# Kernel optimization log

Hardware: AMD Instinct MI355X
Metric: run time of the kernel (lower is better)

Reference implementation:

```python
import jax, jax.numpy as jnp
import numpy as np

B, T, D, H = 4, 4096, 1024, 1024

def log_g(x):
    # log of g(x) = where(x>=0, x+0.5, sigmoid(x)), computed stably in log-space
    return jnp.where(x >= 0, jnp.log(jax.nn.relu(x) + 0.5), -jax.nn.softplus(-x))

def setup_inputs() -> dict:
    key = jax.random.key(0)
    ks = jax.random.split(key, 8)
    s = 1.0 / np.sqrt(D)
    return {
        "x":   jax.random.normal(ks[0], (B, T, D), dtype=jnp.float32),
        "h_0": jax.random.normal(ks[1], (B, H),    dtype=jnp.float32),
        "Wf":  jax.random.uniform(ks[2], (H, D), minval=-s, maxval=s, dtype=jnp.float32),
        "bf":  jax.random.uniform(ks[3], (H,),   minval=-s, maxval=s, dtype=jnp.float32),
        "Wi":  jax.random.uniform(ks[4], (H, D), minval=-s, maxval=s, dtype=jnp.float32),
        "bi":  jax.random.uniform(ks[5], (H,),   minval=-s, maxval=s, dtype=jnp.float32),
        "Wh":  jax.random.uniform(ks[6], (H, D), minval=-s, maxval=s, dtype=jnp.float32),
        "bh":  jax.random.uniform(ks[7], (H,),   minval=-s, maxval=s, dtype=jnp.float32),
    }

def reference(x, h_0, Wf, bf, Wi, bi, Wh, bh):
    # Gate pre-activations: (B, T, H)
    zf = jnp.einsum('btd,hd->bth', x, Wf) + bf
    zi = jnp.einsum('btd,hd->bth', x, Wi) + bi
    zh = jnp.einsum('btd,hd->bth', x, Wh) + bh

    # Normalized gates in log space: log f' = -softplus(diff), log i' = -softplus(-diff)
    diff = jax.nn.softplus(-zf) - jax.nn.softplus(-zi)
    log_f = -jax.nn.softplus(diff)
    log_i = -jax.nn.softplus(-diff)
    log_tilde_h = log_g(zh)

    log_h0 = log_g(h_0)[:, None, :]                               # (B, 1, H)
    log_values = jnp.concatenate([log_h0, log_i + log_tilde_h], axis=1)  # (B, T+1, H)

    # Log-space parallel scan: h_t = f_t h_{t-1} + v_t
    a_star = jnp.cumsum(log_f, axis=1)                            # (B, T, H)
    a_star_pad = jnp.pad(a_star, ((0, 0), (1, 0), (0, 0)))        # (B, T+1, H)
    log_h = a_star_pad + jax.lax.cumlogsumexp(log_values - a_star_pad, axis=1)
    return jnp.exp(log_h[:, 1:, :])                               # (B, T, H)
```

## Files before the change

kernel.cpp:

```cpp
#include <hip/hip_runtime.h>
#include <stdint.h>

#define BB 4
#define TT 4096
#define DD 1024
#define HH 1024
#define MM (BB * TT)
#define NC 128
#define CL (TT / NC)

typedef __bf16 bf16x8 __attribute__((ext_vector_type(8)));
typedef short  s16x8  __attribute__((ext_vector_type(8)));
typedef float  f32x4  __attribute__((ext_vector_type(4)));
typedef float  f32x16 __attribute__((ext_vector_type(16)));


__device__ __forceinline__ unsigned short f2bf(float f) {
    unsigned u = __float_as_uint(f);
    u += 0x7fffu + ((u >> 16) & 1u);
    return (unsigned short)(u >> 16);
}

__device__ __forceinline__ float bf2f(unsigned short u) {
    return __uint_as_float(((unsigned)u) << 16);
}

__device__ __forceinline__ float g_fn(float x) {
    return (x >= 0.f) ? (x + 0.5f) : 1.0f / (1.0f + __expf(-x));
}

__device__ __forceinline__ f32x16 mfma32(s16x8 a, s16x8 b, f32x16 c) {
    return __builtin_amdgcn_mfma_f32_32x32x16_bf16(
        __builtin_bit_cast(bf16x8, a), __builtin_bit_cast(bf16x8, b), c, 0, 0, 0);
}

__device__ __forceinline__ void async_copy16(const void* gsrc, void* ldst) {
    __builtin_amdgcn_global_load_lds(
        reinterpret_cast<__attribute__((address_space(1))) unsigned int*>(
            reinterpret_cast<uintptr_t>(gsrc)),
        reinterpret_cast<__attribute__((address_space(3))) unsigned int*>(
            reinterpret_cast<uintptr_t>(ldst)),
        16, 0, 0);
}


__global__ void cast_all(const float* __restrict__ x,
                         const float* __restrict__ Wf,
                         const float* __restrict__ Wi,
                         const float* __restrict__ Wh,
                         unsigned short* __restrict__ xb,
                         unsigned short* __restrict__ Wb) {
    const int NX = MM * DD / 4;
    int i = blockIdx.x * 256 + threadIdx.x;
    if (i < NX) {
        float4 v = reinterpret_cast<const float4*>(x)[i];
        ushort4 o;
        o.x = f2bf(v.x); o.y = f2bf(v.y); o.z = f2bf(v.z); o.w = f2bf(v.w);
        reinterpret_cast<ushort4*>(xb)[i] = o;
    } else {
        int j = i - NX;
        if (j < 3 * 262144) {
            int which = j >> 18, k = j & 262143;
            const float* s = (which == 0) ? Wf : ((which == 1) ? Wi : Wh);
            float4 v = reinterpret_cast<const float4*>(s)[k];
            ushort4 o;
            o.x = f2bf(v.x); o.y = f2bf(v.y); o.z = f2bf(v.z); o.w = f2bf(v.w);
            reinterpret_cast<ushort4*>(Wb)[(which << 18) + k] = o;
        }
    }
}


#define ISSUE(NB) do {                                                        \
    _Pragma("unroll")                                                         \
    for (int j = 0; j < 4; ++j)                                               \
        async_copy16(sbA[j] + voff, smem + (NB) * 16384 + ldsA[j]);           \
    _Pragma("unroll")                                                         \
    for (int j = 0; j < 3; ++j)                                               \
        async_copy16(sbB[j] + voff, smem + 32768 + (NB) * 12288 + ldsB[j]);   \
    voff += 32;                                                               \
} while (0)

#define COMPUTE(CB) do {                                                      \
    const char* Ab = smem + (CB) * 16384;                                     \
    const char* Bb = smem + 32768 + (CB) * 12288;                             \
    _Pragma("unroll")                                                         \
    for (int ks = 0; ks < 2; ++ks) {                                          \
        const int col = c0 ^ (ks << 5);                                       \
        s16x8 a0 = *reinterpret_cast<const s16x8*>(Ab + arowb + col);         \
        s16x8 a1 = *reinterpret_cast<const s16x8*>(Ab + arowb + 2048 + col);  \
        s16x8 a2 = *reinterpret_cast<const s16x8*>(Ab + arowb + 4096 + col);  \
        s16x8 a3 = *reinterpret_cast<const s16x8*>(Ab + arowb + 6144 + col);  \
        s16x8 b0 = *reinterpret_cast<const s16x8*>(Bb + browb + col);         \
        s16x8 b1 = *reinterpret_cast<const s16x8*>(Bb + browb + 4096 + col);  \
        s16x8 b2 = *reinterpret_cast<const s16x8*>(Bb + browb + 8192 + col);  \
        acc[0][0] = mfma32(a0, b0, acc[0][0]);                                \
        acc[1][0] = mfma32(a0, b1, acc[1][0]);                                \
        acc[2][0] = mfma32(a0, b2, acc[2][0]);                                \
        acc[0][1] = mfma32(a1, b0, acc[0][1]);                                \
        acc[1][1] = mfma32(a1, b1, acc[1][1]);                                \
        acc[2][1] = mfma32(a1, b2, acc[2][1]);                                \
        acc[0][2] = mfma32(a2, b0, acc[0][2]);                                \
        acc[1][2] = mfma32(a2, b1, acc[1][2]);                                \
        acc[2][2] = mfma32(a2, b2, acc[2][2]);                                \
        acc[0][3] = mfma32(a3, b0, acc[0][3]);                                \
        acc[1][3] = mfma32(a3, b1, acc[1][3]);                                \
        acc[2][3] = mfma32(a3, b2, acc[2][3]);                                \
    }                                                                         \
} while (0)

#define STEP(CB, NB, LAST) do {                                               \
    if (!(LAST)) {                                                            \
        ISSUE(NB);                                                            \
        asm volatile("s_waitcnt vmcnt(7)" ::: "memory");                      \
    } else {                                                                  \
        asm volatile("s_waitcnt vmcnt(0)" ::: "memory");                      \
    }                                                                         \
    __builtin_amdgcn_s_barrier();                                             \
    COMPUTE(CB);                                                              \
    asm volatile("s_waitcnt lgkmcnt(0)" ::: "memory");                        \
    __builtin_amdgcn_s_barrier();                                             \
} while (0)

__global__ __launch_bounds__(256, 2) void gemm_gates(
    const unsigned short* __restrict__ xb,
    const unsigned short* __restrict__ Wb,
    const float* __restrict__ bf_p, const float* __restrict__ bi_p,
    const float* __restrict__ bh_p,
    unsigned short* __restrict__ F, unsigned short* __restrict__ V) {
    __shared__ char smem[57344];

    const int tid  = threadIdx.x;
    const int lane = tid & 63;
    const int wub  = __builtin_amdgcn_readfirstlane(tid >> 6);

    const int bi  = blockIdx.x;
    const int xcd = bi & 7;
    const int jj  = bi >> 3;
    const int bm  = ((jj & 7) << 3) | xcd;
    const int bh  = jj >> 3;

    const int pm   = wub >> 1;
    const int ph   = wub & 1;

    int voff = (lane >> 2) * DD +
               (((lane & 3) ^ ((lane >> 3) & 3) ^ ((lane >> 5) & 1)) << 3);

    const unsigned short* sbA[4];
    const unsigned short* sbB[3];
    int ldsA[4], ldsB[3];
#pragma unroll
    for (int j = 0; j < 4; ++j) {
        int s = wub + j * 4;
        sbA[j]  = xb + (size_t)(bm * 256 + s * 16) * DD;
        ldsA[j] = s * 1024;
    }
#pragma unroll
    for (int j = 0; j < 3; ++j) {
        int s = wub + j * 4;
        sbB[j]  = Wb + (size_t)((s >> 2) * HH + bh * 64 + (s & 3) * 16) * DD;
        ldsB[j] = s * 1024;
    }

    const int c0 = ((((lane >> 5) & 1) ^ ((lane >> 1) & 3) ^ ((lane >> 3) & 1)) << 4);
    const int arowb = (pm * 128 + (lane & 31)) * 64;
    const int browb = (ph * 32 + (lane & 31)) * 64;

    f32x16 acc[3][4];
#pragma unroll
    for (int g = 0; g < 3; ++g)
#pragma unroll
        for (int mt = 0; mt < 4; ++mt)
            acc[g][mt] = (f32x16)(0.f);

    ISSUE(0);
    for (int t = 0; t < 15; ++t) {
        STEP(0, 1, 0);
        STEP(1, 0, 0);
    }
    STEP(0, 1, 0);
    STEP(1, 0, 1);

    const int h   = bh * 64 + ph * 32 + (lane & 31);
    const float bfs = bf_p[h], bis = bi_p[h], bhs = bh_p[h];
    const int mb  = bm * 256 + pm * 128 + ((lane >> 5) << 2);
#pragma unroll
    for (int mt = 0; mt < 4; ++mt) {
#pragma unroll
        for (int r = 0; r < 16; ++r) {
            const int m = mb + mt * 32 + (r & 3) + ((r >> 2) << 3);
            float zf = acc[0][mt][r] + bfs;
            float zi = acc[1][mt][r] + bis;
            float zh = acc[2][mt][r] + bhs;
            float ea = __expf(fminf(-zf, 60.f));
            float eb = __expf(fminf(-zi, 60.f));
            float s  = __builtin_amdgcn_rcpf(2.f + ea + eb);
            float fv = (1.f + eb) * s;
            float iv = (1.f + ea) * s;
            float gg = (zh >= 0.f) ? (zh + 0.5f)
                                   : __builtin_amdgcn_rcpf(1.f + __expf(-zh));
            size_t o = (size_t)m * HH + h;
            F[o] = f2bf(fv);
            V[o] = f2bf(iv * gg);
        }
    }
}


__global__ void scan1_kernel(const unsigned short* __restrict__ F,
                             const unsigned short* __restrict__ V,
                             float* __restrict__ Fc, float* __restrict__ Vc) {
    const int bx = blockIdx.x, tid = threadIdx.x;
    const int c = bx & (NC - 1), b = bx >> 7;
    const ushort4* F4 = (const ushort4*)F;
    const ushort4* V4 = (const ushort4*)V;
    size_t base = ((size_t)(b * TT + c * CL) * HH) / 4 + tid;
    float4 Fp = {1.f, 1.f, 1.f, 1.f}, hv = {0.f, 0.f, 0.f, 0.f};
#pragma unroll 8
    for (int s = 0; s < CL; ++s) {
        ushort4 fu = F4[base + (size_t)s * (HH / 4)];
        ushort4 vu = V4[base + (size_t)s * (HH / 4)];
        hv.x = fmaf(bf2f(fu.x), hv.x, bf2f(vu.x)); Fp.x *= bf2f(fu.x);
        hv.y = fmaf(bf2f(fu.y), hv.y, bf2f(vu.y)); Fp.y *= bf2f(fu.y);
        hv.z = fmaf(bf2f(fu.z), hv.z, bf2f(vu.z)); Fp.z *= bf2f(fu.z);
        hv.w = fmaf(bf2f(fu.w), hv.w, bf2f(vu.w)); Fp.w *= bf2f(fu.w);
    }
    size_t ci = ((size_t)(b * NC + c) * HH) / 4 + tid;
    ((float4*)Fc)[ci] = Fp;
    ((float4*)Vc)[ci] = hv;
}

__global__ void scan2_kernel(const float* __restrict__ h0,
                             const float* __restrict__ Fc,
                             const float* __restrict__ Vc,
                             float* __restrict__ Hin) {
    const int gid = blockIdx.x * 256 + threadIdx.x;
    const int b = gid >> 10, h = gid & (HH - 1);
    float carry = g_fn(h0[gid]);
#pragma unroll 8
    for (int c = 0; c < NC; ++c) {
        int ci = (b * NC + c) * HH + h;
        Hin[ci] = carry;
        carry = fmaf(Fc[ci], carry, Vc[ci]);
    }
}

__global__ void scan3_kernel(const unsigned short* __restrict__ F,
                             const unsigned short* __restrict__ V,
                             const float* __restrict__ Hin,
                             float* __restrict__ Out) {
    const int bx = blockIdx.x, tid = threadIdx.x;
    const int c = bx & (NC - 1), b = bx >> 7;
    const ushort4* F4 = (const ushort4*)F;
    const ushort4* V4 = (const ushort4*)V;
    float4* O4 = (float4*)Out;
    size_t base = ((size_t)(b * TT + c * CL) * HH) / 4 + tid;
    size_t ci = ((size_t)(b * NC + c) * HH) / 4 + tid;
    float4 carry = ((const float4*)Hin)[ci];
#pragma unroll 8
    for (int s = 0; s < CL; ++s) {
        size_t idx = base + (size_t)s * (HH / 4);
        ushort4 fu = F4[idx];
        ushort4 vu = V4[idx];
        carry.x = fmaf(bf2f(fu.x), carry.x, bf2f(vu.x));
        carry.y = fmaf(bf2f(fu.y), carry.y, bf2f(vu.y));
        carry.z = fmaf(bf2f(fu.z), carry.z, bf2f(vu.z));
        carry.w = fmaf(bf2f(fu.w), carry.w, bf2f(vu.w));
        O4[idx] = carry;
    }
}


extern "C" void kernel_launch(void* const* d_in, const int* in_sizes, int n_in,
                              void* d_out, int out_size, void* d_ws, size_t ws_size,
                              hipStream_t stream) {
    const float* x   = (const float*)d_in[0];
    const float* h0  = (const float*)d_in[1];
    const float* Wf  = (const float*)d_in[2];
    const float* bfp = (const float*)d_in[3];
    const float* Wi  = (const float*)d_in[4];
    const float* bip = (const float*)d_in[5];
    const float* Wh  = (const float*)d_in[6];
    const float* bhp = (const float*)d_in[7];
    float* out = (float*)d_out;

    char* ws = (char*)d_ws;
    unsigned short* xb = (unsigned short*)ws;
    unsigned short* Wb = (unsigned short*)(ws + 33554432);
    unsigned short* Fb = (unsigned short*)(ws + 39845888);
    unsigned short* Vb = (unsigned short*)(ws + 73400320);
    float* Fc  = (float*)(ws);
    float* Vc  = (float*)(ws + 2097152);
    float* Hin = (float*)(ws + 4194304);

    cast_all<<<19456, 256, 0, stream>>>(x, Wf, Wi, Wh, xb, Wb);
    gemm_gates<<<1024, 256, 0, stream>>>(xb, Wb, bfp, bip, bhp, Fb, Vb);
    scan1_kernel<<<BB * NC, 256, 0, stream>>>(Fb, Vb, Fc, Vc);
    scan2_kernel<<<16, 256, 0, stream>>>(h0, Fc, Vc, Hin);
    scan3_kernel<<<BB * NC, 256, 0, stream>>>(Fb, Vb, Hin, out);
}
```

Baseline: 285.7 us.

## Load weight fragments directly from global memory in MFMA-ready layout, bypassing LDS

The bf16 conversion kernel now writes the three weight matrices in a pre-swizzled layout matching the MFMA B-operand fragment order. The GEMM kernel loads B fragments straight from global memory into registers each k-step instead of staging them through shared memory. This cuts LDS traffic and footprint (57KB down to 32KB), which may allow more occupancy. The cost is more per-wave global/L2 loads of the weights (duplicated across waves) and changed vmcnt accounting, which risks stalls if latency is not hidden.

```diff
diff --git a/kernel.cpp b/kernel.cpp
--- a/kernel.cpp
+++ b/kernel.cpp
@@ -65,7 +65,11 @@
             float4 v = reinterpret_cast<const float4*>(s)[k];
             ushort4 o;
             o.x = f2bf(v.x); o.y = f2bf(v.y); o.z = f2bf(v.z); o.w = f2bf(v.w);
-            reinterpret_cast<ushort4*>(Wb)[(which << 18) + k] = o;
+            int E = k << 2;
+            int h = E >> 10, d = E & 1023;
+            int kb = d >> 5, q = (d >> 3) & 3, e = d & 7;
+            int off = kb * 98304 + q * 24576 + which * 8192 + h * 8 + e;
+            reinterpret_cast<ushort4*>(Wb)[off >> 2] = o;
         }
     }
 }
@@ -75,49 +79,49 @@
     _Pragma("unroll")                                                         \
     for (int j = 0; j < 4; ++j)                                               \
         async_copy16(sbA[j] + voff, smem + (NB) * 16384 + ldsA[j]);           \
-    _Pragma("unroll")                                                         \
-    for (int j = 0; j < 3; ++j)                                               \
-        async_copy16(sbB[j] + voff, smem + 32768 + (NB) * 12288 + ldsB[j]);   \
     voff += 32;                                                               \
 } while (0)
 
-#define COMPUTE(CB) do {                                                      \
-    const char* Ab = smem + (CB) * 16384;                                     \
-    const char* Bb = smem + 32768 + (CB) * 12288;                             \
+#define STEP(CB, NB, LAST) do {                                               \
+    s16x8 bq[2][3];                                                           \
     _Pragma("unroll")                                                         \
-    for (int ks = 0; ks < 2; ++ks) {                                          \
-        const int col = c0 ^ (ks << 5);                                       \
-        s16x8 a0 = *reinterpret_cast<const s16x8*>(Ab + arowb + col);         \
-        s16x8 a1 = *reinterpret_cast<const s16x8*>(Ab + arowb + 2048 + col);  \
-        s16x8 a2 = *reinterpret_cast<const s16x8*>(Ab + arowb + 4096 + col);  \
-        s16x8 a3 = *reinterpret_cast<const s16x8*>(Ab + arowb + 6144 + col);  \
-        s16x8 b0 = *reinterpret_cast<const s16x8*>(Bb + browb + col);         \
-        s16x8 b1 = *reinterpret_cast<const s16x8*>(Bb + browb + 4096 + col);  \
-        s16x8 b2 = *reinterpret_cast<const s16x8*>(Bb + browb + 8192 + col);  \
-        acc[0][0] = mfma32(a0, b0, acc[0][0]);                                \
-        acc[1][0] = mfma32(a0, b1, acc[1][0]);                                \
-        acc[2][0] = mfma32(a0, b2, acc[2][0]);                                \
-        acc[0][1] = mfma32(a1, b0, acc[0][1]);                                \
-        acc[1][1] = mfma32(a1, b1, acc[1][1]);                                \
-        acc[2][1] = mfma32(a1, b2, acc[2][1]);                                \
-        acc[0][2] = mfma32(a2, b0, acc[0][2]);                                \
-        acc[1][2] = mfma32(a2, b1, acc[1][2]);                                \
-        acc[2][2] = mfma32(a2, b2, acc[2][2]);                                \
-        acc[0][3] = mfma32(a3, b0, acc[0][3]);                                \
-        acc[1][3] = mfma32(a3, b1, acc[1][3]);                                \
-        acc[2][3] = mfma32(a3, b2, acc[2][3]);                                \
-    }                                                                         \
-} while (0)
-
-#define STEP(CB, NB, LAST) do {                                               \
+    for (int ks = 0; ks < 2; ++ks)                                            \
+        _Pragma("unroll")                                                     \
+        for (int g = 0; g < 3; ++g)                                           \
+            bq[ks][g] = *reinterpret_cast<const s16x8*>(                      \
+                wp + ks * 49152 + g * 8192);                                  \
+    wp += 98304;                                                              \
+    asm volatile("" ::: "memory");            \
     if (!(LAST)) {                                                            \
         ISSUE(NB);                                                            \
-        asm volatile("s_waitcnt vmcnt(7)" ::: "memory");                      \
+        asm volatile("s_waitcnt vmcnt(10)" ::: "memory");                     \
     } else {                                                                  \
-        asm volatile("s_waitcnt vmcnt(0)" ::: "memory");                      \
+        asm volatile("s_waitcnt vmcnt(6)" ::: "memory");                      \
     }                                                                         \
     __builtin_amdgcn_s_barrier();                                             \
-    COMPUTE(CB);                                                              \
+    {                                                                         \
+        const char* Ab = smem + (CB) * 16384;                                 \
+        _Pragma("unroll")                                                     \
+        for (int ks = 0; ks < 2; ++ks) {                                      \
+            const int col = c0 ^ (ks << 5);                                   \
+            s16x8 a0 = *reinterpret_cast<const s16x8*>(Ab + arowb + col);     \
+            s16x8 a1 = *reinterpret_cast<const s16x8*>(Ab + arowb + 2048 + col); \
+            s16x8 a2 = *reinterpret_cast<const s16x8*>(Ab + arowb + 4096 + col); \
+            s16x8 a3 = *reinterpret_cast<const s16x8*>(Ab + arowb + 6144 + col); \
+            acc[0][0] = mfma32(a0, bq[ks][0], acc[0][0]);                     \
+            acc[1][0] = mfma32(a0, bq[ks][1], acc[1][0]);                     \
+            acc[2][0] = mfma32(a0, bq[ks][2], acc[2][0]);                     \
+            acc[0][1] = mfma32(a1, bq[ks][0], acc[0][1]);                     \
+            acc[1][1] = mfma32(a1, bq[ks][1], acc[1][1]);                     \
+            acc[2][1] = mfma32(a1, bq[ks][2], acc[2][1]);                     \
+            acc[0][2] = mfma32(a2, bq[ks][0], acc[0][2]);                     \
+            acc[1][2] = mfma32(a2, bq[ks][1], acc[1][2]);                     \
+            acc[2][2] = mfma32(a2, bq[ks][2], acc[2][2]);                     \
+            acc[0][3] = mfma32(a3, bq[ks][0], acc[0][3]);                     \
+            acc[1][3] = mfma32(a3, bq[ks][1], acc[1][3]);                     \
+            acc[2][3] = mfma32(a3, bq[ks][2], acc[2][3]);                     \
+        }                                                                     \
+    }                                                                         \
     asm volatile("s_waitcnt lgkmcnt(0)" ::: "memory");                        \
     __builtin_amdgcn_s_barrier();                                             \
 } while (0)
@@ -128,7 +132,7 @@
     const float* __restrict__ bf_p, const float* __restrict__ bi_p,
     const float* __restrict__ bh_p,
     unsigned short* __restrict__ F, unsigned short* __restrict__ V) {
-    __shared__ char smem[57344];
+    __shared__ char smem[32768];
 
     const int tid  = threadIdx.x;
     const int lane = tid & 63;
@@ -147,24 +151,19 @@
                (((lane & 3) ^ ((lane >> 3) & 3) ^ ((lane >> 5) & 1)) << 3);
 
     const unsigned short* sbA[4];
-    const unsigned short* sbB[3];
-    int ldsA[4], ldsB[3];
+    int ldsA[4];
 #pragma unroll
     for (int j = 0; j < 4; ++j) {
         int s = wub + j * 4;
         sbA[j]  = xb + (size_t)(bm * 256 + s * 16) * DD;
         ldsA[j] = s * 1024;
     }
-#pragma unroll
-    for (int j = 0; j < 3; ++j) {
-        int s = wub + j * 4;
-        sbB[j]  = Wb + (size_t)((s >> 2) * HH + bh * 64 + (s & 3) * 16) * DD;
-        ldsB[j] = s * 1024;
-    }
+
+    const unsigned short* wp = Wb + (lane >> 5) * 24576 +
+                               (size_t)(bh * 64 + ph * 32 + (lane & 31)) * 8;
 
     const int c0 = ((((lane >> 5) & 1) ^ ((lane >> 1) & 3) ^ ((lane >> 3) & 1)) << 4);
     const int arowb = (pm * 128 + (lane & 31)) * 64;
-    const int browb = (ph * 32 + (lane & 31)) * 64;
 
     f32x16 acc[3][4];
 #pragma unroll
```

After: 292.3 us. 2.3% more time.
